# Optimization experiments

Measured on AMD Instinct MI355X. Metric: run time of the kernel, lower is better.

## Reference

```python
import jax, jax.numpy as jnp
import numpy as np

B, L, HID, H, DH = 1, 2048, 1024, 16, 64
KW = 2  # d_conv
EPS = float(np.finfo(np.float32).eps)  # torch RMSNorm eps=None -> dtype eps


def _causal_dw_conv(x, w, b):
    # x: (B, L, D), w: (D, K), b: (D,). Depthwise causal conv, no activation.
    Bs, Ls, D = x.shape
    K = w.shape[1]
    xp = jnp.pad(x, ((0, 0), (K - 1, 0), (0, 0)))
    out = b
    for k in range(K):
        out = out + xp[:, k:k + Ls, :] * w[:, k]
    return out


def setup_inputs() -> dict:
    key = jax.random.key(0)
    ks = jax.random.split(key, 14)
    hidden_states = jax.random.normal(ks[0], (B, L, HID), jnp.float32)
    # masked_fill(attention_mask != 0, -inf): True above diagonal (future masked)
    attention_mask = jnp.triu(jnp.ones((L, L), dtype=bool), 1)[None, None]
    all_dim = 3 * H * DH  # q_size + 2*kv_size with KVH == H
    qkv_w = jax.random.normal(ks[1], (all_dim, HID), jnp.float32) * 0.02
    q_conv_w = jax.random.normal(ks[2], (H * DH, KW), jnp.float32) * 0.5
    q_conv_b = jax.random.normal(ks[3], (H * DH,), jnp.float32) * 0.02
    k_conv_w = jax.random.normal(ks[4], (H * DH, KW), jnp.float32) * 0.5
    k_conv_b = jax.random.normal(ks[5], (H * DH,), jnp.float32) * 0.02
    v_conv_w = jax.random.normal(ks[6], (H * DH, KW), jnp.float32) * 0.5
    v_conv_b = jax.random.normal(ks[7], (H * DH,), jnp.float32) * 0.02
    norm_w = jnp.ones((DH,), jnp.float32)
    A_log = jnp.log(jax.random.uniform(ks[8], (H,), jnp.float32, 1.0, 16.0))
    dt0 = jnp.exp(jax.random.uniform(ks[9], (H,), jnp.float32)
                  * (np.log(0.1) - np.log(0.001)) + np.log(0.001))
    dt0 = jnp.clip(dt0, 1e-4)
    dt_bias = dt0 + jnp.log(-jnp.expm1(-dt0))  # inverse softplus init
    dt_proj_w = jax.random.normal(ks[10], (H, HID), jnp.float32) * 0.02
    dt_proj_b = jnp.zeros((H,), jnp.float32)
    o_w = jax.random.normal(ks[11], (HID, H * DH), jnp.float32) * 0.02
    order_coeff = jnp.ones((1, H, 1, 1), jnp.float32)  # 1/cumprod(arange(1,2))
    return dict(hidden_states=hidden_states, attention_mask=attention_mask,
                qkv_w=qkv_w, q_conv_w=q_conv_w, q_conv_b=q_conv_b,
                k_conv_w=k_conv_w, k_conv_b=k_conv_b, v_conv_w=v_conv_w,
                v_conv_b=v_conv_b, norm_w=norm_w, A_log=A_log, dt_bias=dt_bias,
                dt_proj_w=dt_proj_w, dt_proj_b=dt_proj_b, o_w=o_w,
                order_coeff=order_coeff)


def reference(hidden_states, attention_mask, qkv_w, q_conv_w, q_conv_b,
              k_conv_w, k_conv_b, v_conv_w, v_conv_b, norm_w, A_log, dt_bias,
              dt_proj_w, dt_proj_b, o_w, order_coeff):
    qs = H * DH
    qkv = hidden_states @ qkv_w.T                    # (B, L, 3*H*DH)
    q = _causal_dw_conv(qkv[..., :qs], q_conv_w, q_conv_b)
    k = _causal_dw_conv(qkv[..., qs:2 * qs], k_conv_w, k_conv_b)
    v = _causal_dw_conv(qkv[..., 2 * qs:], v_conv_w, v_conv_b)
    # split heads -> (B, H, L, DH)
    q = q.reshape(B, L, H, DH).transpose(0, 2, 1, 3)
    k = k.reshape(B, L, H, DH).transpose(0, 2, 1, 3)
    v = v.reshape(B, L, H, DH).transpose(0, 2, 1, 3)
    # SSM-style gate: dt (B, L, H)
    dt = jax.nn.softplus(hidden_states @ dt_proj_w.T + dt_proj_b + dt_bias)
    v = v * jnp.swapaxes(dt, 1, 2)[..., None]        # value scaled by dt
    A = -jnp.exp(A_log)[None, None, :] * dt          # (B, L, H)
    A_cumsum = jnp.swapaxes(jnp.cumsum(A, axis=1), 1, 2)  # (B, H, L)
    diff = A_cumsum[:, :, :, None] - A_cumsum[:, :, None, :]  # (B, H, L, L)
    A_mask = jnp.exp(jnp.where(attention_mask, -jnp.inf, diff))
    # order == 1: Taylor series reduces to a single gated linear term
    scores = jnp.einsum('bhld,bhmd->bhlm', q, k) * A_mask * (1.0 / order_coeff)
    out = scores @ v                                  # (B, H, L, DH)
    # RMSNorm over head_dim
    out = out * jax.lax.rsqrt(jnp.mean(out * out, -1, keepdims=True) + EPS) * norm_w
    out = out.transpose(0, 2, 1, 3).reshape(B, L, H * DH)
    return out @ o_w.T
```

## Files before the change

### kernel.cpp

```cpp
#include <hip/hip_runtime.h>
#include <hip/hip_bf16.h>

#define L_SEQ 2048
#define HIDN  1024
#define NH    16
#define DHD   64
#define QKV_P 3200
#define QC_S  2048

typedef float f4 __attribute__((ext_vector_type(4)));
typedef __bf16 bf16x8 __attribute__((ext_vector_type(8)));
typedef _Float16 half8 __attribute__((ext_vector_type(8)));
typedef unsigned int u32x2 __attribute__((ext_vector_type(2)));

union H8 {
  half8 h;
  u32x2 u2[2];
  uint4 u4;
};

__device__ __forceinline__ float b2f(unsigned short u) {
  union { unsigned int i; float f; } c; c.i = ((unsigned int)u) << 16; return c.f;
}
__device__ __forceinline__ unsigned short f2b(float f) {
  union { float f; unsigned int i; } c; c.f = f;
  unsigned int r = c.i + 0x7FFFu + ((c.i >> 16) & 1u);
  return (unsigned short)(r >> 16);
}
__device__ __forceinline__ unsigned short f2h(float f) {
  union { _Float16 h; unsigned short u; } c; c.h = (_Float16)f; return c.u;
}

__global__ __launch_bounds__(256) void prep_kernel(
    const void* hs, const void* qkvw, const void* ow, const void* dtw,
    const void* qw, const void* qb, const void* kw, const void* kb,
    const void* vw, const void* vb, const void* nw, const void* al,
    const void* dtb, const void* dpb, const void* oc,
    unsigned short* __restrict__ hs_b, unsigned short* __restrict__ qkvw_b,
    unsigned short* __restrict__ ow_b,
    float* __restrict__ smallf, int* __restrict__ flag)
{
  __shared__ int cnt;
  if (threadIdx.x == 0) cnt = 0;
  __syncthreads();
  {
    const unsigned short* p = (const unsigned short*)hs;
    int c = 0;
    for (int i = threadIdx.x; i < 8192; i += 256)
      if (((p[i] >> 7) & 0xFFu) >= 140u) c++;
    atomicAdd(&cnt, c);
  }
  __syncthreads();
  const int f = (cnt >= 32) ? 1 : 0;
  if (blockIdx.x == 0 && threadIdx.x == 0) *flag = f;

  const int tid = blockIdx.x * 256 + threadIdx.x;
  const int nth = gridDim.x * 256;
  for (int i = tid; i < 1605632; i += nth) {
    const void* src; unsigned short* dst; int off;
    if (i < 524288)       { src = hs;   dst = hs_b;   off = i; }
    else if (i < 1310720) { src = qkvw; dst = qkvw_b; off = i - 524288; }
    else if (i < 1314816) { src = dtw;  dst = qkvw_b + 3072 * 1024; off = i - 1310720; }
    else if (i < 1343488) {
      *(ushort4*)(qkvw_b + 3088 * 1024 + (i - 1314816) * 4) = (ushort4){0, 0, 0, 0};
      continue;
    }
    else                  { src = ow;   dst = ow_b;   off = i - 1343488; }
    const int e = off * 4;
    if (f) {
      f4 v = *(const f4*)((const float*)src + e);
      ushort4 o;
      o.x = f2b(v[0]); o.y = f2b(v[1]); o.z = f2b(v[2]); o.w = f2b(v[3]);
      *(ushort4*)(dst + e) = o;
    } else {
      *(uint2*)(dst + e) = *(const uint2*)((const unsigned short*)src + e);
    }
  }
  const void* ptrs[11] = {qw, qb, kw, kb, vw, vb, nw, al, dtb, dpb, oc};
  const int sizes[11] = {2048, 1024, 2048, 1024, 2048, 1024, 64, 16, 16, 16, 16};
  int off = 0;
  for (int a = 0; a < 11; ++a) {
    for (int i = tid; i < sizes[a]; i += nth)
      smallf[off + i] = f ? ((const float*)ptrs[a])[i]
                          : b2f(((const unsigned short*)ptrs[a])[i]);
    off += sizes[a];
  }
}

__global__ __launch_bounds__(256) void gemm128(
    const unsigned short* __restrict__ A, const unsigned short* __restrict__ B,
    float* __restrict__ C, int M, int N, int K)
{
  __shared__ __align__(16) unsigned short As[128 * 40];
  __shared__ __align__(16) unsigned short Bs[128 * 40];
  const int t = threadIdx.x;
  const int w = t >> 6, lane = t & 63;
  const int quad = lane >> 4, l16 = lane & 15;
  const int wr = w >> 1, wc = w & 1;
  const int m0 = blockIdx.y * 128, n0 = blockIdx.x * 128;
  const int srow = t >> 1;
  const int scol = (t & 1) * 16;

  f4 acc[4][4];
#pragma unroll
  for (int i = 0; i < 4; ++i)
#pragma unroll
    for (int j = 0; j < 4; ++j) acc[i][j] = (f4){0.f, 0.f, 0.f, 0.f};

  const unsigned short* apg = A + (size_t)(m0 + srow) * K + scol;
  const unsigned short* bpg = B + (size_t)(n0 + srow) * K + scol;
  uint4 a0 = *(const uint4*)apg,       a1 = *(const uint4*)(apg + 8);
  uint4 b0 = *(const uint4*)bpg,       b1 = *(const uint4*)(bpg + 8);

  for (int k0 = 0; k0 < K; k0 += 32) {
    __syncthreads();
    *(uint4*)&As[srow * 40 + scol]     = a0;
    *(uint4*)&As[srow * 40 + scol + 8] = a1;
    *(uint4*)&Bs[srow * 40 + scol]     = b0;
    *(uint4*)&Bs[srow * 40 + scol + 8] = b1;
    __syncthreads();
    if (k0 + 32 < K) {
      a0 = *(const uint4*)(apg + k0 + 32); a1 = *(const uint4*)(apg + k0 + 40);
      b0 = *(const uint4*)(bpg + k0 + 32); b1 = *(const uint4*)(bpg + k0 + 40);
    }
    bf16x8 aF[4], bF[4];
#pragma unroll
    for (int i = 0; i < 4; ++i)
      aF[i] = *(const bf16x8*)&As[(wr * 64 + i * 16 + l16) * 40 + quad * 8];
#pragma unroll
    for (int j = 0; j < 4; ++j)
      bF[j] = *(const bf16x8*)&Bs[(wc * 64 + j * 16 + l16) * 40 + quad * 8];
#pragma unroll
    for (int i = 0; i < 4; ++i)
#pragma unroll
      for (int j = 0; j < 4; ++j)
        acc[i][j] = __builtin_amdgcn_mfma_f32_16x16x32_bf16(aF[i], bF[j], acc[i][j], 0, 0, 0);
  }

#pragma unroll
  for (int i = 0; i < 4; ++i)
#pragma unroll
    for (int j = 0; j < 4; ++j)
#pragma unroll
      for (int r = 0; r < 4; ++r) {
        int m = m0 + wr * 64 + i * 16 + quad * 4 + r;
        int n = n0 + wc * 64 + j * 16 + l16;
        C[(size_t)m * N + n] = acc[i][j][r];
      }
}

template <int MODE>
__global__ __launch_bounds__(256) void gemm_bt(
    const unsigned short* __restrict__ A, const unsigned short* __restrict__ B,
    void* __restrict__ Cv, int M, int N, int K, const int* __restrict__ flag)
{
  __shared__ __align__(16) short As[64 * 40];
  __shared__ __align__(16) short Bs[64 * 40];
  const int t = threadIdx.x;
  const int wave = t >> 6, lane = t & 63;
  const int quad = lane >> 4, l16 = lane & 15;
  const int m0 = blockIdx.y * 64, n0 = blockIdx.x * 64;
  const int srow = t >> 2, scol = (t & 3) * 8;
  f4 acc[4];
#pragma unroll
  for (int i = 0; i < 4; ++i) acc[i] = (f4){0.f, 0.f, 0.f, 0.f};
  const unsigned short* ap = A + (size_t)(m0 + srow) * K + scol;
  const unsigned short* bp = B + (size_t)(n0 + srow) * K + scol;
  for (int k0 = 0; k0 < K; k0 += 32) {
    uint4 av = *(const uint4*)(ap + k0);
    uint4 bv = *(const uint4*)(bp + k0);
    __syncthreads();
    *(uint4*)&As[srow * 40 + scol] = av;
    *(uint4*)&Bs[srow * 40 + scol] = bv;
    __syncthreads();
    bf16x8 af = *(const bf16x8*)&As[(wave * 16 + l16) * 40 + quad * 8];
#pragma unroll
    for (int nt = 0; nt < 4; ++nt) {
      bf16x8 bf = *(const bf16x8*)&Bs[(nt * 16 + l16) * 40 + quad * 8];
      acc[nt] = __builtin_amdgcn_mfma_f32_16x16x32_bf16(af, bf, acc[nt], 0, 0, 0);
    }
  }
  const int outf32 = (MODE == 0) ? 1 : (*flag ? 1 : 0);
#pragma unroll
  for (int nt = 0; nt < 4; ++nt) {
#pragma unroll
    for (int r = 0; r < 4; ++r) {
      int m = m0 + wave * 16 + quad * 4 + r;
      int n = n0 + nt * 16 + l16;
      if (outf32) ((float*)Cv)[(size_t)m * N + n] = acc[nt][r];
      else        ((unsigned short*)Cv)[(size_t)m * N + n] = f2b(acc[nt][r]);
    }
  }
}

__global__ __launch_bounds__(64) void cumsum_kernel(
    const float* __restrict__ qkvf, const float* __restrict__ smallf,
    float* __restrict__ dt_out, float* __restrict__ Ac)
{
  const int h = blockIdx.x;
  const int lane = threadIdx.x;
  const int base = lane * 32;
  const float dpb = smallf[9312 + h], dtb = smallf[9296 + h];
  const float nal = -expf(smallf[9280 + h]);
  float Av[32];
  float run = 0.f;
#pragma unroll
  for (int i = 0; i < 32; ++i) {
    const int l = base + i;
    float z = qkvf[(size_t)l * QKV_P + 3072 + h] + dpb + dtb;
    float dtv = (z > 20.f) ? z : log1pf(expf(z));
    dt_out[l * NH + h] = dtv;
    Av[i] = nal * dtv;
    run += Av[i];
  }
  float incl = run;
#pragma unroll
  for (int off = 1; off < 64; off <<= 1) {
    float n = __shfl_up(incl, off);
    if (lane >= off) incl += n;
  }
  float r2 = incl - run;
#pragma unroll
  for (int i = 0; i < 32; ++i) {
    r2 += Av[i];
    Ac[h * L_SEQ + base + i] = r2;
  }
}

__global__ __launch_bounds__(256) void conv_kernel(
    const float* __restrict__ qkvf, const float* __restrict__ smallf,
    const float* __restrict__ dt, unsigned short* __restrict__ qc,
    unsigned short* __restrict__ vt)
{
  if (blockIdx.x < 4096) {
    const int idx = blockIdx.x * 256 + threadIdx.x;
    const int l = idx >> 9;
    const int c = (idx & 511) * 4;
    f4 xc = *(const f4*)&qkvf[(size_t)l * QKV_P + c];
    f4 xp = (f4){0.f, 0.f, 0.f, 0.f};
    if (l > 0) xp = *(const f4*)&qkvf[(size_t)(l - 1) * QKV_P + c];
    const float* w; const float* b; int cb;
    if (c < HIDN) { w = smallf;        b = smallf + 2048; cb = c; }
    else          { w = smallf + 3072; b = smallf + 5120; cb = c - HIDN; }
    f4 o;
#pragma unroll
    for (int j = 0; j < 4; ++j)
      o[j] = b[cb + j] + xp[j] * w[(cb + j) * 2] + xc[j] * w[(cb + j) * 2 + 1];
    ushort4 st;
    st.x = f2h(o[0]); st.y = f2h(o[1]); st.z = f2h(o[2]); st.w = f2h(o[3]);
    *(ushort4*)&qc[(size_t)l * QC_S + c] = st;
  } else {
    __shared__ __align__(16) unsigned short Ts[64 * 68];
    const int bv = blockIdx.x - 4096;
    const int h = bv & 15;
    const int lt0 = bv >> 4;
    const int t = threadIdx.x;
    const int srow = t >> 2, cc = t & 3;
    const int l = lt0 * 64 + srow;
    const int cb = h * 64 + cc * 16;
    const float* w = smallf + 6144;
    const float* b = smallf + 8192;
    const float dtv = dt[l * NH + h];
    const float* xcp = &qkvf[(size_t)l * QKV_P + 2048 + cb];
    const float* xpp = &qkvf[(size_t)(l - 1) * QKV_P + 2048 + cb];
    unsigned short o16[16];
#pragma unroll
    for (int g = 0; g < 4; ++g) {
      f4 xc = *(const f4*)(xcp + g * 4);
      f4 xp = (f4){0.f, 0.f, 0.f, 0.f};
      if (l > 0) xp = *(const f4*)(xpp + g * 4);
#pragma unroll
      for (int j = 0; j < 4; ++j) {
        const int ch = cb + g * 4 + j;
        float o = b[ch] + xp[j] * w[ch * 2] + xc[j] * w[ch * 2 + 1];
        o16[g * 4 + j] = f2h(o * dtv);
      }
    }
    *(uint4*)&Ts[srow * 68 + cc * 16]     = *(const uint4*)&o16[0];
    *(uint4*)&Ts[srow * 68 + cc * 16 + 8] = *(const uint4*)&o16[8];
    __syncthreads();
    __align__(16) unsigned short o[16];
#pragma unroll
    for (int j = 0; j < 16; ++j) o[j] = Ts[(cc * 16 + j) * 68 + srow];
    unsigned short* op = vt + ((size_t)h * DHD + srow) * L_SEQ + lt0 * 64 + cc * 16;
    *(uint4*)op = *(const uint4*)&o[0];
    *(uint4*)(op + 8) = *(const uint4*)&o[8];
  }
}

__global__ __launch_bounds__(256) void attn_kernel(
    const unsigned short* __restrict__ qc,
    const unsigned short* __restrict__ vt,
    const float* __restrict__ Ac,
    const float* __restrict__ smallf,
    unsigned short* __restrict__ attn_out)
{
  const int n  = blockIdx.x + 32 * blockIdx.y;
  const int q_ = n >> 3;
  const int h  = (n & 7) + 8 * (q_ & 1);
  const int bxw = q_ >> 1;
  const int lt = (bxw < 16) ? bxw : (47 - bxw);
  const int t  = threadIdx.x;
  const int w    = t >> 6;
  const int lane = t & 63;
  const int l16  = lane & 15;
  const int quad = lane >> 4;
  const int srow = t >> 2;
  const int cc   = t & 3;

  __shared__ __align__(16) unsigned short K_lds[2][64 * 68];
  __shared__ __align__(16) unsigned short V_lds[2][64 * 68];
  __shared__ __align__(16) unsigned short S_lds[64 * 68];

  const int l0 = lt * 64;
  const float rc = 1.0f / smallf[9328 + h];
  const float* Acp = Ac + h * L_SEQ;

  H8 qf0, qf1;
  {
    const unsigned short* qp =
        qc + (size_t)(l0 + w * 16 + l16) * QC_S + h * DHD + quad * 8;
    qf0.u4 = *(const uint4*)qp;
    qf1.u4 = *(const uint4*)(qp + 32);
  }
  float alv[4];
#pragma unroll
  for (int r = 0; r < 4; ++r) alv[r] = Acp[l0 + w * 16 + quad * 4 + r];

  f4 acc[4];
#pragma unroll
  for (int i = 0; i < 4; ++i) acc[i] = (f4){0.f, 0.f, 0.f, 0.f};

  const unsigned short* kgp =
      qc + (size_t)srow * QC_S + HIDN + h * DHD + cc * 16;
  const unsigned short* vgp =
      vt + ((size_t)h * DHD + srow) * L_SEQ + cc * 16;

  const int swo = srow * 68 + cc * 16;

  uint4 k0v = *(const uint4*)kgp,       k1v = *(const uint4*)(kgp + 8);
  uint4 v0v = *(const uint4*)vgp,       v1v = *(const uint4*)(vgp + 8);
  float amv[4];
#pragma unroll
  for (int nt = 0; nt < 4; ++nt) amv[nt] = Acp[nt * 16 + l16];

  *(u32x2*)&K_lds[0][swo]      = (u32x2){k0v.x, k0v.y};
  *(u32x2*)&K_lds[0][swo + 4]  = (u32x2){k0v.z, k0v.w};
  *(u32x2*)&K_lds[0][swo + 8]  = (u32x2){k1v.x, k1v.y};
  *(u32x2*)&K_lds[0][swo + 12] = (u32x2){k1v.z, k1v.w};
  *(u32x2*)&V_lds[0][swo]      = (u32x2){v0v.x, v0v.y};
  *(u32x2*)&V_lds[0][swo + 4]  = (u32x2){v0v.z, v0v.w};
  *(u32x2*)&V_lds[0][swo + 8]  = (u32x2){v1v.x, v1v.y};
  *(u32x2*)&V_lds[0][swo + 12] = (u32x2){v1v.z, v1v.w};
  __syncthreads();

  int cur = 0;
  for (int it = 0; it <= lt; ++it) {
    uint4 nk0 = k0v, nk1 = k1v, nv0 = v0v, nv1 = v1v;
    float namv[4];
    const bool more = (it < lt);
    if (more) {
      const unsigned short* kp = kgp + (size_t)(it + 1) * 64 * QC_S;
      const unsigned short* vp = vgp + (size_t)(it + 1) * 64;
      nk0 = *(const uint4*)kp; nk1 = *(const uint4*)(kp + 8);
      nv0 = *(const uint4*)vp; nv1 = *(const uint4*)(vp + 8);
#pragma unroll
      for (int nt = 0; nt < 4; ++nt)
        namv[nt] = Acp[(it + 1) * 64 + nt * 16 + l16];
    }

    f4 s[4];
#pragma unroll
    for (int i = 0; i < 4; ++i) s[i] = (f4){0.f, 0.f, 0.f, 0.f};
#pragma unroll
    for (int ks = 0; ks < 2; ++ks) {
      H8 qk = ks ? qf1 : qf0;
#pragma unroll
      for (int nt = 0; nt < 4; ++nt) {
        H8 kf;
        const int ko = (nt * 16 + l16) * 68 + ks * 32 + quad * 8;
        kf.u2[0] = *(const u32x2*)&K_lds[cur][ko];
        kf.u2[1] = *(const u32x2*)&K_lds[cur][ko + 4];
        s[nt] = __builtin_amdgcn_mfma_f32_16x16x32_f16(qk.h, kf.h, s[nt], 0, 0, 0);
      }
    }
    const int m0 = it * 64;
#pragma unroll
    for (int nt = 0; nt < 4; ++nt) {
      const int mg = m0 + nt * 16 + l16;
      const float am = amv[nt];
#pragma unroll
      for (int r = 0; r < 4; ++r) {
        const int lg = l0 + w * 16 + quad * 4 + r;
        float val = (mg <= lg) ? s[nt][r] * __expf(alv[r] - am) * rc : 0.0f;
        S_lds[(w * 16 + quad * 4 + r) * 68 + nt * 16 + l16] = f2h(val);
      }
    }
#pragma unroll
    for (int ks = 0; ks < 2; ++ks) {
      H8 sa;
      const int so = (w * 16 + l16) * 68 + ks * 32 + quad * 8;
      sa.u2[0] = *(const u32x2*)&S_lds[so];
      sa.u2[1] = *(const u32x2*)&S_lds[so + 4];
#pragma unroll
      for (int db = 0; db < 4; ++db) {
        H8 vb;
        const int vo = (db * 16 + l16) * 68 + ks * 32 + quad * 8;
        vb.u2[0] = *(const u32x2*)&V_lds[cur][vo];
        vb.u2[1] = *(const u32x2*)&V_lds[cur][vo + 4];
        acc[db] = __builtin_amdgcn_mfma_f32_16x16x32_f16(sa.h, vb.h, acc[db], 0, 0, 0);
      }
    }
    if (more) {
      unsigned short* Kl = K_lds[cur ^ 1];
      unsigned short* Vl = V_lds[cur ^ 1];
      *(u32x2*)&Kl[swo]      = (u32x2){nk0.x, nk0.y};
      *(u32x2*)&Kl[swo + 4]  = (u32x2){nk0.z, nk0.w};
      *(u32x2*)&Kl[swo + 8]  = (u32x2){nk1.x, nk1.y};
      *(u32x2*)&Kl[swo + 12] = (u32x2){nk1.z, nk1.w};
      *(u32x2*)&Vl[swo]      = (u32x2){nv0.x, nv0.y};
      *(u32x2*)&Vl[swo + 4]  = (u32x2){nv0.z, nv0.w};
      *(u32x2*)&Vl[swo + 8]  = (u32x2){nv1.x, nv1.y};
      *(u32x2*)&Vl[swo + 12] = (u32x2){nv1.z, nv1.w};
#pragma unroll
      for (int nt = 0; nt < 4; ++nt) amv[nt] = namv[nt];
      __syncthreads();
      cur ^= 1;
    }
  }

#pragma unroll
  for (int r = 0; r < 4; ++r) {
    float p = acc[0][r] * acc[0][r] + acc[1][r] * acc[1][r]
            + acc[2][r] * acc[2][r] + acc[3][r] * acc[3][r];
#pragma unroll
    for (int off = 1; off < 16; off <<= 1) p += __shfl_xor(p, off);
    const float rn = rsqrtf(p * (1.0f / 64.0f) + 1.1920928955078125e-07f);
    unsigned short* op =
        attn_out + (size_t)(l0 + w * 16 + quad * 4 + r) * HIDN + h * DHD + l16;
#pragma unroll
    for (int ds = 0; ds < 4; ++ds)
      op[ds * 16] = f2b(acc[ds][r] * rn * smallf[9216 + ds * 16 + l16]);
  }
}

extern "C" void kernel_launch(void* const* d_in, const int* in_sizes, int n_in,
                              void* d_out, int out_size, void* d_ws, size_t ws_size,
                              hipStream_t stream)
{
  (void)in_sizes; (void)n_in; (void)out_size; (void)ws_size;
  const void* hs        = d_in[0];
  const void* qkv_w     = d_in[2];
  const void* q_conv_w  = d_in[3];
  const void* q_conv_b  = d_in[4];
  const void* k_conv_w  = d_in[5];
  const void* k_conv_b  = d_in[6];
  const void* v_conv_w  = d_in[7];
  const void* v_conv_b  = d_in[8];
  const void* norm_w    = d_in[9];
  const void* A_log     = d_in[10];
  const void* dt_bias   = d_in[11];
  const void* dt_proj_w = d_in[12];
  const void* dt_proj_b = d_in[13];
  const void* o_w       = d_in[14];
  const void* ordc      = d_in[15];

  char* ws = (char*)d_ws;
  int* flag             = (int*)ws;
  unsigned short* hs_b  = (unsigned short*)(ws + 256);
  unsigned short* qkvw_b= (unsigned short*)(ws + 4194560);
  unsigned short* ow_b  = (unsigned short*)(ws + 10748160);
  float* smallf         = (float*)(ws + 12845312);
  float* qkvf           = (float*)(ws + 12882688);
  unsigned short* qc_h  = (unsigned short*)(ws + 39097088);
  float* dtbuf          = (float*)(ws + 47485696);
  float* Acum           = (float*)(ws + 47616768);
  unsigned short* attnb = (unsigned short*)(ws + 47747840);
  unsigned short* vt_h  = (unsigned short*)(ws + 51942144);

  prep_kernel<<<1024, 256, 0, stream>>>(
      hs, qkv_w, o_w, dt_proj_w,
      q_conv_w, q_conv_b, k_conv_w, k_conv_b, v_conv_w, v_conv_b,
      norm_w, A_log, dt_bias, dt_proj_b, ordc,
      hs_b, qkvw_b, ow_b, smallf, flag);

  gemm128<<<dim3(QKV_P / 128, L_SEQ / 128), 256, 0, stream>>>(
      hs_b, qkvw_b, qkvf, L_SEQ, QKV_P, HIDN);
  cumsum_kernel<<<NH, 64, 0, stream>>>(qkvf, smallf, dtbuf, Acum);
  conv_kernel<<<4096 + 512, 256, 0, stream>>>(qkvf, smallf, dtbuf, qc_h, vt_h);
  attn_kernel<<<dim3(32, NH), 256, 0, stream>>>(qc_h, vt_h, Acum, smallf, attnb);
  gemm_bt<1><<<dim3(HIDN / 64, L_SEQ / 64), 256, 0, stream>>>(
      attnb, ow_b, d_out, L_SEQ, HIDN, HIDN, flag);
}
```

Before: 247.3 us.

## Split attention key range across two blocks and add reduce kernel

The attention kernel now splits each query tile's causal key range into two halves handled by separate blocks, which doubles the grid to 1024 blocks. Each block writes fp32 partial outputs, and a new reduce kernel sums the halves and applies the RMSNorm. K and V are now loaded straight from global memory into MFMA register fragments instead of being staged in double-buffered LDS, which removes the per-iteration barriers. In exchange it adds an extra launch, an fp32 partial-output round trip through memory, and uncoalesced per-lane global loads.

```diff
diff --git a/kernel.cpp b/kernel.cpp
--- a/kernel.cpp
+++ b/kernel.cpp
@@ -293,23 +293,26 @@
     const unsigned short* __restrict__ vt,
     const float* __restrict__ Ac,
     const float* __restrict__ smallf,
-    unsigned short* __restrict__ attn_out)
-{
-  const int n  = blockIdx.x + 32 * blockIdx.y;
+    float* __restrict__ po)
+{
+  const int n  = blockIdx.x;
+  const int r_ = n & 7;
   const int q_ = n >> 3;
-  const int h  = (n & 7) + 8 * (q_ & 1);
-  const int bxw = q_ >> 1;
-  const int lt = (bxw < 16) ? bxw : (47 - bxw);
+  const int hh = q_ & 1;
+  const int s_ = (q_ >> 1) & 1;
+  const int u  = q_ >> 2;
+  const int h  = r_ + 8 * hh;
+  const int lt = (u < 16) ? u : (47 - u);
+  const int nT = lt + 1;
+  const int mStart = s_ ? ((nT + 1) >> 1) : 0;
+  const int mEnd   = s_ ? nT : ((nT + 1) >> 1);
+
   const int t  = threadIdx.x;
   const int w    = t >> 6;
   const int lane = t & 63;
   const int l16  = lane & 15;
   const int quad = lane >> 4;
-  const int srow = t >> 2;
-  const int cc   = t & 3;
-
-  __shared__ __align__(16) unsigned short K_lds[2][64 * 68];
-  __shared__ __align__(16) unsigned short V_lds[2][64 * 68];
+
   __shared__ __align__(16) unsigned short S_lds[64 * 68];
 
   const int l0 = lt * 64;
@@ -331,42 +334,39 @@
 #pragma unroll
   for (int i = 0; i < 4; ++i) acc[i] = (f4){0.f, 0.f, 0.f, 0.f};
 
-  const unsigned short* kgp =
-      qc + (size_t)srow * QC_S + HIDN + h * DHD + cc * 16;
-  const unsigned short* vgp =
-      vt + ((size_t)h * DHD + srow) * L_SEQ + cc * 16;
-
-  const int swo = srow * 68 + cc * 16;
-
-  uint4 k0v = *(const uint4*)kgp,       k1v = *(const uint4*)(kgp + 8);
-  uint4 v0v = *(const uint4*)vgp,       v1v = *(const uint4*)(vgp + 8);
-  float amv[4];
-#pragma unroll
-  for (int nt = 0; nt < 4; ++nt) amv[nt] = Acp[nt * 16 + l16];
-
-  *(u32x2*)&K_lds[0][swo]      = (u32x2){k0v.x, k0v.y};
-  *(u32x2*)&K_lds[0][swo + 4]  = (u32x2){k0v.z, k0v.w};
-  *(u32x2*)&K_lds[0][swo + 8]  = (u32x2){k1v.x, k1v.y};
-  *(u32x2*)&K_lds[0][swo + 12] = (u32x2){k1v.z, k1v.w};
-  *(u32x2*)&V_lds[0][swo]      = (u32x2){v0v.x, v0v.y};
-  *(u32x2*)&V_lds[0][swo + 4]  = (u32x2){v0v.z, v0v.w};
-  *(u32x2*)&V_lds[0][swo + 8]  = (u32x2){v1v.x, v1v.y};
-  *(u32x2*)&V_lds[0][swo + 12] = (u32x2){v1v.z, v1v.w};
-  __syncthreads();
-
-  int cur = 0;
-  for (int it = 0; it <= lt; ++it) {
-    uint4 nk0 = k0v, nk1 = k1v, nv0 = v0v, nv1 = v1v;
-    float namv[4];
-    const bool more = (it < lt);
+  const unsigned short* kbase = qc + HIDN + h * DHD + quad * 8 + (size_t)l16 * QC_S;
+  const unsigned short* vbase = vt + ((size_t)(h * DHD + l16)) * L_SEQ + quad * 8;
+
+  uint4 kc[8];
+  if (mStart < mEnd) {
+    const int m0 = mStart * 64;
+#pragma unroll
+    for (int f = 0; f < 8; ++f) {
+      const int nt = f & 3, ks = f >> 2;
+      kc[f] = *(const uint4*)(kbase + (size_t)(m0 + nt * 16) * QC_S + ks * 32);
+    }
+  }
+
+  for (int mt = mStart; mt < mEnd; ++mt) {
+    const int m0 = mt * 64;
+    uint4 vc[8];
+#pragma unroll
+    for (int f = 0; f < 8; ++f) {
+      const int db = f & 3, ks = f >> 2;
+      vc[f] = *(const uint4*)(vbase + (size_t)(db * 16) * L_SEQ + m0 + ks * 32);
+    }
+    float amv[4];
+#pragma unroll
+    for (int nt = 0; nt < 4; ++nt) amv[nt] = Acp[m0 + nt * 16 + l16];
+    uint4 kn[8];
+    const bool more = (mt + 1 < mEnd);
     if (more) {
-      const unsigned short* kp = kgp + (size_t)(it + 1) * 64 * QC_S;
-      const unsigned short* vp = vgp + (size_t)(it + 1) * 64;
-      nk0 = *(const uint4*)kp; nk1 = *(const uint4*)(kp + 8);
-      nv0 = *(const uint4*)vp; nv1 = *(const uint4*)(vp + 8);
-#pragma unroll
-      for (int nt = 0; nt < 4; ++nt)
-        namv[nt] = Acp[(it + 1) * 64 + nt * 16 + l16];
+      const int m1 = m0 + 64;
+#pragma unroll
+      for (int f = 0; f < 8; ++f) {
+        const int nt = f & 3, ks = f >> 2;
+        kn[f] = *(const uint4*)(kbase + (size_t)(m1 + nt * 16) * QC_S + ks * 32);
+      }
     }
 
     f4 s[4];
@@ -377,14 +377,10 @@
       H8 qk = ks ? qf1 : qf0;
 #pragma unroll
       for (int nt = 0; nt < 4; ++nt) {
-        H8 kf;
-        const int ko = (nt * 16 + l16) * 68 + ks * 32 + quad * 8;
-        kf.u2[0] = *(const u32x2*)&K_lds[cur][ko];
-        kf.u2[1] = *(const u32x2*)&K_lds[cur][ko + 4];
+        H8 kf; kf.u4 = kc[ks * 4 + nt];
         s[nt] = __builtin_amdgcn_mfma_f32_16x16x32_f16(qk.h, kf.h, s[nt], 0, 0, 0);
       }
     }
-    const int m0 = it * 64;
 #pragma unroll
     for (int nt = 0; nt < 4; ++nt) {
       const int mg = m0 + nt * 16 + l16;
@@ -404,44 +400,49 @@
       sa.u2[1] = *(const u32x2*)&S_lds[so + 4];
 #pragma unroll
       for (int db = 0; db < 4; ++db) {
-        H8 vb;
-        const int vo = (db * 16 + l16) * 68 + ks * 32 + quad * 8;
-        vb.u2[0] = *(const u32x2*)&V_lds[cur][vo];
-        vb.u2[1] = *(const u32x2*)&V_lds[cur][vo + 4];
+        H8 vb; vb.u4 = vc[ks * 4 + db];
         acc[db] = __builtin_amdgcn_mfma_f32_16x16x32_f16(sa.h, vb.h, acc[db], 0, 0, 0);
       }
     }
     if (more) {
-      unsigned short* Kl = K_lds[cur ^ 1];
-      unsigned short* Vl = V_lds[cur ^ 1];
-      *(u32x2*)&Kl[swo]      = (u32x2){nk0.x, nk0.y};
-      *(u32x2*)&Kl[swo + 4]  = (u32x2){nk0.z, nk0.w};
-      *(u32x2*)&Kl[swo + 8]  = (u32x2){nk1.x, nk1.y};
-      *(u32x2*)&Kl[swo + 12] = (u32x2){nk1.z, nk1.w};
-      *(u32x2*)&Vl[swo]      = (u32x2){nv0.x, nv0.y};
-      *(u32x2*)&Vl[swo + 4]  = (u32x2){nv0.z, nv0.w};
-      *(u32x2*)&Vl[swo + 8]  = (u32x2){nv1.x, nv1.y};
-      *(u32x2*)&Vl[swo + 12] = (u32x2){nv1.z, nv1.w};
-#pragma unroll
-      for (int nt = 0; nt < 4; ++nt) amv[nt] = namv[nt];
-      __syncthreads();
-      cur ^= 1;
-    }
-  }
-
+#pragma unroll
+      for (int f = 0; f < 8; ++f) kc[f] = kn[f];
+    }
+  }
+
+  float* pout = po + (size_t)s_ * (L_SEQ * HIDN);
 #pragma unroll
   for (int r = 0; r < 4; ++r) {
-    float p = acc[0][r] * acc[0][r] + acc[1][r] * acc[1][r]
-            + acc[2][r] * acc[2][r] + acc[3][r] * acc[3][r];
-#pragma unroll
-    for (int off = 1; off < 16; off <<= 1) p += __shfl_xor(p, off);
-    const float rn = rsqrtf(p * (1.0f / 64.0f) + 1.1920928955078125e-07f);
-    unsigned short* op =
-        attn_out + (size_t)(l0 + w * 16 + quad * 4 + r) * HIDN + h * DHD + l16;
-#pragma unroll
-    for (int ds = 0; ds < 4; ++ds)
-      op[ds * 16] = f2b(acc[ds][r] * rn * smallf[9216 + ds * 16 + l16]);
-  }
+    float* op = pout + (size_t)(l0 + w * 16 + quad * 4 + r) * HIDN + h * DHD + l16;
+#pragma unroll
+    for (int db = 0; db < 4; ++db)
+      op[db * 16] = acc[db][r];
+  }
+}
+
+__global__ __launch_bounds__(256) void reduce_kernel(
+    const float* __restrict__ po, const float* __restrict__ smallf,
+    unsigned short* __restrict__ attn_out)
+{
+  const int l = blockIdx.x;
+  const int t = threadIdx.x;
+  const int col = t * 4;
+  const float* p0 = po + (size_t)l * HIDN + col;
+  const float* p1 = p0 + (size_t)L_SEQ * HIDN;
+  f4 a = *(const f4*)p0;
+  f4 b = *(const f4*)p1;
+  f4 o = a + b;
+  float p = o[0] * o[0] + o[1] * o[1] + o[2] * o[2] + o[3] * o[3];
+#pragma unroll
+  for (int off = 1; off < 16; off <<= 1) p += __shfl_xor(p, off);
+  const float rn = rsqrtf(p * (1.0f / 64.0f) + 1.1920928955078125e-07f);
+  const int d0 = col & 63;
+  ushort4 st;
+  st.x = f2b(o[0] * rn * smallf[9216 + d0]);
+  st.y = f2b(o[1] * rn * smallf[9216 + d0 + 1]);
+  st.z = f2b(o[2] * rn * smallf[9216 + d0 + 2]);
+  st.w = f2b(o[3] * rn * smallf[9216 + d0 + 3]);
+  *(ushort4*)&attn_out[(size_t)l * HIDN + col] = st;
 }
 
 extern "C" void kernel_launch(void* const* d_in, const int* in_sizes, int n_in,
@@ -477,6 +478,7 @@
   float* Acum           = (float*)(ws + 47616768);
   unsigned short* attnb = (unsigned short*)(ws + 47747840);
   unsigned short* vt_h  = (unsigned short*)(ws + 51942144);
+  float* po             = (float*)(ws + 56136448);
 
   prep_kernel<<<1024, 256, 0, stream>>>(
       hs, qkv_w, o_w, dt_proj_w,
@@ -488,7 +490,8 @@
       hs_b, qkvw_b, qkvf, L_SEQ, QKV_P, HIDN);
   cumsum_kernel<<<NH, 64, 0, stream>>>(qkvf, smallf, dtbuf, Acum);
   conv_kernel<<<4096 + 512, 256, 0, stream>>>(qkvf, smallf, dtbuf, qc_h, vt_h);
-  attn_kernel<<<dim3(32, NH), 256, 0, stream>>>(qc_h, vt_h, Acum, smallf, attnb);
+  attn_kernel<<<1024, 256, 0, stream>>>(qc_h, vt_h, Acum, smallf, po);
+  reduce_kernel<<<L_SEQ, 256, 0, stream>>>(po, smallf, attnb);
   gemm_bt<1><<<dim3(HIDN / 64, L_SEQ / 64), 256, 0, stream>>>(
       attnb, ow_b, d_out, L_SEQ, HIDN, HIDN, flag);
 }
```

After: 274.9 us. +11.1%, slower.
